# Kernel optimization log

Measured on AMD Instinct MI355X. Metric: run time of the kernel, lower is better.

## Reference

```python
import jax, jax.numpy as jnp
import numpy as np

D_MODEL, D_K, D_V, N_HEADS = 1024, 64, 64, 16
B, S = 8, 1024
NEG = -1e9
LN_EPS = 1e-5


def setup_inputs() -> dict:
    key = jax.random.key(0)
    ks = jax.random.split(key, 10)
    scale = 1.0 / np.sqrt(D_MODEL)
    return {
        "Q_in": jax.random.normal(ks[0], (B, S, D_MODEL), jnp.float32),
        "K_in": jax.random.normal(ks[1], (B, S, D_MODEL), jnp.float32),
        "V_in": jax.random.normal(ks[2], (B, S, D_MODEL), jnp.float32),
        "mask": jax.random.randint(ks[3], (B, S, S), 0, 2).astype(bool),
        "W_Q": jax.random.normal(ks[4], (D_MODEL, N_HEADS * D_K), jnp.float32) * scale,
        "W_K": jax.random.normal(ks[5], (D_MODEL, N_HEADS * D_K), jnp.float32) * scale,
        "W_V": jax.random.normal(ks[6], (D_MODEL, N_HEADS * D_V), jnp.float32) * scale,
        "W_fc": jax.random.normal(ks[7], (N_HEADS * D_V, D_MODEL), jnp.float32) * scale,
        "ln_gamma": jnp.ones((D_MODEL,), jnp.float32),
        "ln_beta": jnp.zeros((D_MODEL,), jnp.float32),
    }


def reference(Q_in, K_in, V_in, mask, W_Q, W_K, W_V, W_fc, ln_gamma, ln_beta):
    b = Q_in.shape[0]
    # projections -> (B, H, S, d)
    Q = (Q_in @ W_Q).reshape(b, -1, N_HEADS, D_K).transpose(0, 2, 1, 3)
    K = (K_in @ W_K).reshape(b, -1, N_HEADS, D_K).transpose(0, 2, 1, 3)
    V = (V_in @ W_V).reshape(b, -1, N_HEADS, D_V).transpose(0, 2, 1, 3)
    # scores (B, H, Sq, Sk)
    scores = jnp.einsum("bhqd,bhkd->bhqk", Q, K) / np.sqrt(D_K)
    scores = jnp.where(mask[:, None, :, :], NEG, scores)
    attn = jax.nn.softmax(scores, axis=-1)
    context = jnp.einsum("bhqk,bhkd->bhqd", attn, V)
    context = context.transpose(0, 2, 1, 3).reshape(b, -1, N_HEADS * D_V)
    out = context @ W_fc + Q_in  # residual
    mu = jnp.mean(out, axis=-1, keepdims=True)
    var = jnp.var(out, axis=-1, keepdims=True)
    out = (out - mu) * jax.lax.rsqrt(var + LN_EPS) * ln_gamma + ln_beta
    return out, attn
```

## Files before the change

### kernel.cpp

```cpp
#include <hip/hip_runtime.h>
#include <stdint.h>

typedef unsigned short u16;
typedef float f32x4 __attribute__((ext_vector_type(4)));
typedef short s16x8 __attribute__((ext_vector_type(8)));

constexpr int B  = 8;
constexpr int S  = 1024;
constexpr int DM = 1024;
constexpr int H  = 16;
constexpr int M  = B * S;
constexpr float NEGINF = -1e9f;

__device__ __forceinline__ u16 f2bf(float f) {
    union { float f; uint32_t u; } v; v.f = f;
    uint32_t u = v.u;
    uint32_t r = 0x7FFFu + ((u >> 16) & 1u);
    return (u16)((u + r) >> 16);
}

__device__ __forceinline__ void gload16(const u16* g, u16* l) {
    __builtin_amdgcn_global_load_lds(
        (const __attribute__((address_space(1))) unsigned int*)g,
        (__attribute__((address_space(3))) unsigned int*)l, 16, 0, 0);
}

__global__ void cvt_all(const float* __restrict__ q, const float* __restrict__ k,
                        const float* __restrict__ v,
                        u16* __restrict__ xq, u16* __restrict__ xk, u16* __restrict__ xv) {
    const float* in; u16* out;
    if (blockIdx.y == 0)      { in = q; out = xq; }
    else if (blockIdx.y == 1) { in = k; out = xk; }
    else                      { in = v; out = xv; }
    int i = (blockIdx.x * 256 + threadIdx.x) * 4;
    float4 val = *(const float4*)(in + i);
    ushort4 o;
    o.x = f2bf(val.x); o.y = f2bf(val.y); o.z = f2bf(val.z); o.w = f2bf(val.w);
    *(ushort4*)(out + i) = o;
}

__global__ void transpose_all(const float* __restrict__ w0, const float* __restrict__ w1,
                              const float* __restrict__ w2, const float* __restrict__ w3,
                              u16* __restrict__ o0, u16* __restrict__ o1,
                              u16* __restrict__ o2, u16* __restrict__ o3) {
    const float* W; u16* Wt;
    switch (blockIdx.z) {
        case 0:  W = w0; Wt = o0; break;
        case 1:  W = w1; Wt = o1; break;
        case 2:  W = w2; Wt = o2; break;
        default: W = w3; Wt = o3; break;
    }
    __shared__ float tile[32][33];
    int n0 = blockIdx.x * 32, k0 = blockIdx.y * 32;
    int tx = threadIdx.x & 31, ty = threadIdx.x >> 5;
#pragma unroll
    for (int r = 0; r < 4; ++r)
        tile[ty + r*8][tx] = W[(size_t)(k0 + ty + r*8) * DM + n0 + tx];
    __syncthreads();
#pragma unroll
    for (int r = 0; r < 4; ++r)
        Wt[(size_t)(n0 + ty + r*8) * DM + k0 + tx] = f2bf(tile[tx][ty + r*8]);
}

template<int EPI>
__global__ __launch_bounds__(256, 2)
void gemm_bt(const u16* __restrict__ A, const u16* __restrict__ Bt,
             void* __restrict__ Cv, const float* __restrict__ resid)
{
    __shared__ u16 As[128 * 32];
    __shared__ u16 Bs[128 * 32];
    const int m0 = blockIdx.y * 128;
    const int n0 = blockIdx.x * 128;
    const int t = threadIdx.x;
    const int lane = t & 63;
    const int wid = t >> 6;
    const int wm = (wid >> 1) * 64;
    const int wn = (wid & 1) * 64;
    const int lr = lane & 15;
    const int lg = lane >> 4;

    const u16* Ag = A  + (size_t)(m0 + (t >> 2)) * 1024 + (t & 3) * 8;
    const u16* Bg = Bt + (size_t)(n0 + (t >> 2)) * 1024 + (t & 3) * 8;
    u16* Al = As + t * 8;
    u16* Bl = Bs + t * 8;

    f32x4 acc[4][4] = {};

    for (int kt = 0; kt < 32; ++kt) {
        const int ko = kt * 32;
        __syncthreads();
        gload16(Ag + ko,            Al);
        gload16(Ag + 64*1024 + ko,  Al + 64*32);
        gload16(Bg + ko,            Bl);
        gload16(Bg + 64*1024 + ko,  Bl + 64*32);
        __syncthreads();
        s16x8 af[4], bfr[4];
#pragma unroll
        for (int m = 0; m < 4; ++m)
            af[m] = *(const s16x8*)(As + (wm + m*16 + lr) * 32 + lg * 8);
#pragma unroll
        for (int n = 0; n < 4; ++n)
            bfr[n] = *(const s16x8*)(Bs + (wn + n*16 + lr) * 32 + lg * 8);
#pragma unroll
        for (int m = 0; m < 4; ++m)
#pragma unroll
            for (int n = 0; n < 4; ++n)
                acc[m][n] = __builtin_amdgcn_mfma_f32_16x16x32_bf16(af[m], bfr[n], acc[m][n], 0, 0, 0);
    }

#pragma unroll
    for (int m = 0; m < 4; ++m) {
#pragma unroll
        for (int n = 0; n < 4; ++n) {
            const int rg0 = m0 + wm + m*16 + lg*4;
            const int cg  = n0 + wn + n*16 + lr;
            if constexpr (EPI == 0) {
                u16* C = (u16*)Cv;
#pragma unroll
                for (int r = 0; r < 4; ++r)
                    C[(size_t)(rg0 + r) * 1024 + cg] = f2bf(acc[m][n][r]);
            } else if constexpr (EPI == 1) {
                u16* C = (u16*)Cv;
                const int bb = rg0 >> 10;
                const int s0 = rg0 & 1023;
                const int hh = cg >> 6;
                const int dd = cg & 63;
                ushort4 pk;
                pk.x = f2bf(acc[m][n][0]); pk.y = f2bf(acc[m][n][1]);
                pk.z = f2bf(acc[m][n][2]); pk.w = f2bf(acc[m][n][3]);
                *(ushort4*)(C + (size_t)((bb*16 + hh)*64 + dd) * 1024 + s0) = pk;
            } else {
                float* C = (float*)Cv;
#pragma unroll
                for (int r = 0; r < 4; ++r) {
                    size_t idx = (size_t)(rg0 + r) * 1024 + cg;
                    C[idx] = acc[m][n][r] + resid[idx];
                }
            }
        }
    }
}

__global__ __launch_bounds__(256, 2)
void attn_fused(const u16* __restrict__ Qp, const u16* __restrict__ Kp,
                const void* __restrict__ maskp, const u16* __restrict__ Vt,
                float* __restrict__ attn, u16* __restrict__ ctx)
{
    const int h  = blockIdx.x;
    const int q0 = blockIdx.y * 32;
    const int b  = blockIdx.z;
    const int t = threadIdx.x;
    const int lane = t & 63;
    const int w = t >> 6;
    const int lr = lane & 15;
    const int lg = lane >> 4;

    constexpr int PLD = 1032;
    __shared__ u16 Plds[32 * PLD];
    __shared__ float redA[4][32];
    __shared__ float redB[4][32];

    uint32_t orv = 0;
    const uint32_t* mw = (const uint32_t*)maskp;
#pragma unroll
    for (int i = 0; i < 64; ++i) orv |= mw[i];
    const bool mask_bytes = (orv > 1u);

    s16x8 qf[2][2];
#pragma unroll
    for (int mq = 0; mq < 2; ++mq)
#pragma unroll
        for (int ks = 0; ks < 2; ++ks)
            qf[mq][ks] = *(const s16x8*)(Qp + (size_t)(b*S + q0 + mq*16 + lr) * DM + h*64 + ks*32 + lg*8);

    f32x4 acc[2][16];
#pragma unroll
    for (int nk = 0; nk < 16; ++nk) {
        const int sk = w*256 + nk*16 + lr;
        const u16* kb = Kp + (size_t)(b*S + sk) * DM + h*64 + lg*8;
        s16x8 kf0 = *(const s16x8*)(kb);
        s16x8 kf1 = *(const s16x8*)(kb + 32);
        f32x4 c0 = {};
        c0 = __builtin_amdgcn_mfma_f32_16x16x32_bf16(qf[0][0], kf0, c0, 0, 0, 0);
        c0 = __builtin_amdgcn_mfma_f32_16x16x32_bf16(qf[0][1], kf1, c0, 0, 0, 0);
        acc[0][nk] = c0;
        f32x4 c1 = {};
        c1 = __builtin_amdgcn_mfma_f32_16x16x32_bf16(qf[1][0], kf0, c1, 0, 0, 0);
        c1 = __builtin_amdgcn_mfma_f32_16x16x32_bf16(qf[1][1], kf1, c1, 0, 0, 0);
        acc[1][nk] = c1;
    }

    const size_t mbase = (size_t)b * S * S;
#pragma unroll
    for (int mq = 0; mq < 2; ++mq) {
#pragma unroll
        for (int r = 0; r < 4; ++r) {
            const int q = q0 + mq*16 + lg*4 + r;
            const size_t roff = mbase + (size_t)q * S + w*256 + lr;
#pragma unroll
            for (int nk = 0; nk < 16; ++nk) {
                int mv;
                if (mask_bytes) mv = ((const uint8_t*)maskp)[roff + nk*16];
                else            mv = ((const int*)maskp)[roff + nk*16];
                float s = acc[mq][nk][r] * 0.125f;
                acc[mq][nk][r] = mv ? NEGINF : s;
            }
        }
    }

    float rmax[2][4];
#pragma unroll
    for (int mq = 0; mq < 2; ++mq)
#pragma unroll
        for (int r = 0; r < 4; ++r) {
            float m = acc[mq][0][r];
#pragma unroll
            for (int nk = 1; nk < 16; ++nk) m = fmaxf(m, acc[mq][nk][r]);
#pragma unroll
            for (int d = 1; d < 16; d <<= 1) m = fmaxf(m, __shfl_xor(m, d, 64));
            rmax[mq][r] = m;
        }
    if (lr == 0) {
#pragma unroll
        for (int mq = 0; mq < 2; ++mq)
#pragma unroll
            for (int r = 0; r < 4; ++r)
                redA[w][mq*16 + lg*4 + r] = rmax[mq][r];
    }
    __syncthreads();
#pragma unroll
    for (int mq = 0; mq < 2; ++mq)
#pragma unroll
        for (int r = 0; r < 4; ++r) {
            const int row = mq*16 + lg*4 + r;
            rmax[mq][r] = fmaxf(fmaxf(redA[0][row], redA[1][row]),
                                fmaxf(redA[2][row], redA[3][row]));
        }

#pragma unroll
    for (int mq = 0; mq < 2; ++mq)
#pragma unroll
        for (int r = 0; r < 4; ++r) {
            float sme = 0.f;
#pragma unroll
            for (int nk = 0; nk < 16; ++nk) {
                float p = __expf(acc[mq][nk][r] - rmax[mq][r]);
                acc[mq][nk][r] = p;
                sme += p;
            }
#pragma unroll
            for (int d = 1; d < 16; d <<= 1) sme += __shfl_xor(sme, d, 64);
            if (lr == 0) redB[w][mq*16 + lg*4 + r] = sme;
        }
    __syncthreads();

#pragma unroll
    for (int mq = 0; mq < 2; ++mq)
#pragma unroll
        for (int r = 0; r < 4; ++r) {
            const int row = mq*16 + lg*4 + r;
            const float inv = 1.0f / (redB[0][row] + redB[1][row] + redB[2][row] + redB[3][row]);
#pragma unroll
            for (int nk = 0; nk < 16; ++nk) {
                float p = acc[mq][nk][r] * inv;
                acc[mq][nk][r] = p;
                Plds[row * PLD + w*256 + nk*16 + lr] = f2bf(p);
            }
        }
    __syncthreads();

    float* ab = attn + (size_t)(b*H + h) * S * S;
#pragma unroll
    for (int mq = 0; mq < 2; ++mq)
#pragma unroll
        for (int r = 0; r < 4; ++r) {
            float* arow = ab + (size_t)(q0 + mq*16 + lg*4 + r) * S + w*256 + lr;
#pragma unroll
            for (int nk = 0; nk < 16; ++nk)
                arow[nk*16] = acc[mq][nk][r];
        }

    const u16* vb = Vt + (size_t)(b*H + h) * 64 * S + (size_t)(w*16 + lr) * S;
    f32x4 pacc[2] = {};
    for (int kt = 0; kt < 32; ++kt) {
        const int k0 = kt*32 + lg*8;
        s16x8 vf = *(const s16x8*)(vb + k0);
#pragma unroll
        for (int mq = 0; mq < 2; ++mq) {
            s16x8 af = *(const s16x8*)(Plds + (mq*16 + lr) * PLD + k0);
            pacc[mq] = __builtin_amdgcn_mfma_f32_16x16x32_bf16(af, vf, pacc[mq], 0, 0, 0);
        }
    }
#pragma unroll
    for (int mq = 0; mq < 2; ++mq)
#pragma unroll
        for (int r = 0; r < 4; ++r)
            ctx[(size_t)(b*S + q0 + mq*16 + lg*4 + r) * DM + h*64 + w*16 + lr] = f2bf(pacc[mq][r]);
}

__global__ __launch_bounds__(256)
void layernorm(const float* __restrict__ x, const float* __restrict__ gamma,
               const float* __restrict__ beta, float* __restrict__ out)
{
    const int row = blockIdx.x;
    const int t = threadIdx.x;
    const float* xr = x + (size_t)row * DM;
    float4 v = *(const float4*)(xr + t*4);
    float s  = v.x + v.y + v.z + v.w;
    float s2 = v.x*v.x + v.y*v.y + v.z*v.z + v.w*v.w;
#pragma unroll
    for (int d = 1; d < 64; d <<= 1) {
        s  += __shfl_xor(s,  d, 64);
        s2 += __shfl_xor(s2, d, 64);
    }
    __shared__ float ls[4], ls2[4];
    if ((t & 63) == 0) { ls[t >> 6] = s; ls2[t >> 6] = s2; }
    __syncthreads();
    s  = ls[0] + ls[1] + ls[2] + ls[3];
    s2 = ls2[0] + ls2[1] + ls2[2] + ls2[3];
    const float mu  = s * (1.0f / DM);
    const float var = s2 * (1.0f / DM) - mu * mu;
    const float rs  = rsqrtf(var + 1e-5f);
    float4 g  = *(const float4*)(gamma + t*4);
    float4 bb = *(const float4*)(beta  + t*4);
    float4 o;
    o.x = (v.x - mu) * rs * g.x + bb.x;
    o.y = (v.y - mu) * rs * g.y + bb.y;
    o.z = (v.z - mu) * rs * g.z + bb.z;
    o.w = (v.w - mu) * rs * g.w + bb.w;
    *(float4*)(out + (size_t)row * DM + t*4) = o;
}

extern "C" void kernel_launch(void* const* d_in, const int* in_sizes, int n_in,
                              void* d_out, int out_size, void* d_ws, size_t ws_size,
                              hipStream_t stream) {
    const float* Qin  = (const float*)d_in[0];
    const float* Kin  = (const float*)d_in[1];
    const float* Vin  = (const float*)d_in[2];
    const void*  mask = d_in[3];
    const float* Wq   = (const float*)d_in[4];
    const float* Wk   = (const float*)d_in[5];
    const float* Wv   = (const float*)d_in[6];
    const float* Wfc  = (const float*)d_in[7];
    const float* gam  = (const float*)d_in[8];
    const float* bet  = (const float*)d_in[9];

    float* out  = (float*)d_out;
    float* attn = (float*)d_out + (size_t)M * DM;

    char* ws = (char*)d_ws;
    constexpr size_t SZ_X = (size_t)M * DM * 2;
    constexpr size_t SZ_W = (size_t)DM * DM * 2;
    u16* Xq  = (u16*)(ws);
    u16* Xk  = (u16*)(ws + SZ_X);
    u16* Xv  = (u16*)(ws + 2*SZ_X);
    u16* WqT = (u16*)(ws + 3*SZ_X);
    u16* WkT = (u16*)(ws + 3*SZ_X + SZ_W);
    u16* WvT = (u16*)(ws + 3*SZ_X + 2*SZ_W);
    u16* WfT = (u16*)(ws + 3*SZ_X + 3*SZ_W);
    u16* Qp  = (u16*)(ws + 3*SZ_X + 4*SZ_W);
    u16* Kp  = (u16*)(ws + 4*SZ_X + 4*SZ_W);
    u16* Vt  = (u16*)(ws + 5*SZ_X + 4*SZ_W);
    float* preLN = (float*)(ws);
    u16*   Ctx   = (u16*)(ws + 2*SZ_X);

    dim3 blk(256);
    cvt_all<<<dim3(M * DM / 1024, 3), blk, 0, stream>>>(Qin, Kin, Vin, Xq, Xk, Xv);
    transpose_all<<<dim3(32, 32, 4), blk, 0, stream>>>(Wq, Wk, Wv, Wfc, WqT, WkT, WvT, WfT);

    gemm_bt<0><<<dim3(8, 64), blk, 0, stream>>>(Xq, WqT, Qp, nullptr);
    gemm_bt<0><<<dim3(8, 64), blk, 0, stream>>>(Xk, WkT, Kp, nullptr);
    gemm_bt<1><<<dim3(8, 64), blk, 0, stream>>>(Xv, WvT, Vt, nullptr);

    attn_fused<<<dim3(H, S / 32, B), blk, 0, stream>>>(Qp, Kp, mask, Vt, attn, Ctx);

    gemm_bt<2><<<dim3(8, 64), blk, 0, stream>>>(Ctx, WfT, preLN, Qin);
    layernorm<<<dim3(M), blk, 0, stream>>>(preLN, gam, bet, out);
}
```

Baseline: 568.3 us.

## Restructure attention block to 16 queries with transposed scores and vectorized stores

Each attention block now handles 16 query rows instead of 32. The score MFMA swaps its operands so each lane holds 4 consecutive key columns, which lets mask reads become uchar4/int4 loads and attn writes become float4 stores instead of scalar strided accesses. P·V is split along the key dimension across the 4 waves, with partial context sums reduced through LDS. LDS use per block drops and the launch bound targets 3 blocks per CU. The cost is that K is re-read twice as often and there is an extra cross-wave reduction step.

Result: faster. 547.0 us (-3.7%).

```diff
diff --git a/kernel.cpp b/kernel.cpp
--- a/kernel.cpp
+++ b/kernel.cpp
@@ -141,13 +141,13 @@
     }
 }
 
-__global__ __launch_bounds__(256, 2)
+__global__ __launch_bounds__(256, 3)
 void attn_fused(const u16* __restrict__ Qp, const u16* __restrict__ Kp,
                 const void* __restrict__ maskp, const u16* __restrict__ Vt,
                 float* __restrict__ attn, u16* __restrict__ ctx)
 {
     const int h  = blockIdx.x;
-    const int q0 = blockIdx.y * 32;
+    const int q0 = blockIdx.y * 16;
     const int b  = blockIdx.z;
     const int t = threadIdx.x;
     const int lane = t & 63;
@@ -155,10 +155,10 @@
     const int lr = lane & 15;
     const int lg = lane >> 4;
 
-    constexpr int PLD = 1032;
-    __shared__ u16 Plds[32 * PLD];
-    __shared__ float redA[4][32];
-    __shared__ float redB[4][32];
+    __shared__ u16  Pl[4][16][264];
+    __shared__ float ctxp[4][16][64];
+    __shared__ float redA[4][16];
+    __shared__ float redB[4][16];
 
     uint32_t orv = 0;
     const uint32_t* mw = (const uint32_t*)maskp;
@@ -166,136 +166,116 @@
     for (int i = 0; i < 64; ++i) orv |= mw[i];
     const bool mask_bytes = (orv > 1u);
 
-    s16x8 qf[2][2];
-#pragma unroll
-    for (int mq = 0; mq < 2; ++mq)
-#pragma unroll
-        for (int ks = 0; ks < 2; ++ks)
-            qf[mq][ks] = *(const s16x8*)(Qp + (size_t)(b*S + q0 + mq*16 + lr) * DM + h*64 + ks*32 + lg*8);
-
-    f32x4 acc[2][16];
+    const u16* qb = Qp + (size_t)(b*S + q0 + lr) * DM + h*64 + lg*8;
+    s16x8 qf0 = *(const s16x8*)(qb);
+    s16x8 qf1 = *(const s16x8*)(qb + 32);
+
+    f32x4 p[16];
 #pragma unroll
     for (int nk = 0; nk < 16; ++nk) {
-        const int sk = w*256 + nk*16 + lr;
-        const u16* kb = Kp + (size_t)(b*S + sk) * DM + h*64 + lg*8;
+        const u16* kb = Kp + (size_t)(b*S + w*256 + nk*16 + lr) * DM + h*64 + lg*8;
         s16x8 kf0 = *(const s16x8*)(kb);
         s16x8 kf1 = *(const s16x8*)(kb + 32);
-        f32x4 c0 = {};
-        c0 = __builtin_amdgcn_mfma_f32_16x16x32_bf16(qf[0][0], kf0, c0, 0, 0, 0);
-        c0 = __builtin_amdgcn_mfma_f32_16x16x32_bf16(qf[0][1], kf1, c0, 0, 0, 0);
-        acc[0][nk] = c0;
-        f32x4 c1 = {};
-        c1 = __builtin_amdgcn_mfma_f32_16x16x32_bf16(qf[1][0], kf0, c1, 0, 0, 0);
-        c1 = __builtin_amdgcn_mfma_f32_16x16x32_bf16(qf[1][1], kf1, c1, 0, 0, 0);
-        acc[1][nk] = c1;
-    }
-
-    const size_t mbase = (size_t)b * S * S;
-#pragma unroll
-    for (int mq = 0; mq < 2; ++mq) {
-#pragma unroll
-        for (int r = 0; r < 4; ++r) {
-            const int q = q0 + mq*16 + lg*4 + r;
-            const size_t roff = mbase + (size_t)q * S + w*256 + lr;
-#pragma unroll
-            for (int nk = 0; nk < 16; ++nk) {
-                int mv;
-                if (mask_bytes) mv = ((const uint8_t*)maskp)[roff + nk*16];
-                else            mv = ((const int*)maskp)[roff + nk*16];
-                float s = acc[mq][nk][r] * 0.125f;
-                acc[mq][nk][r] = mv ? NEGINF : s;
-            }
+        f32x4 c = {};
+        c = __builtin_amdgcn_mfma_f32_16x16x32_bf16(kf0, qf0, c, 0, 0, 0);
+        c = __builtin_amdgcn_mfma_f32_16x16x32_bf16(kf1, qf1, c, 0, 0, 0);
+        p[nk] = c;
+    }
+
+    const size_t mrow = (size_t)b * S * S + (size_t)(q0 + lr) * S;
+#pragma unroll
+    for (int nk = 0; nk < 16; ++nk) {
+        const size_t off = mrow + w*256 + nk*16 + lg*4;
+        int m0, m1, m2, m3;
+        if (mask_bytes) {
+            uchar4 mb = *(const uchar4*)((const uint8_t*)maskp + off);
+            m0 = mb.x; m1 = mb.y; m2 = mb.z; m3 = mb.w;
+        } else {
+            int4 mi = *(const int4*)((const int*)maskp + off);
+            m0 = mi.x; m1 = mi.y; m2 = mi.z; m3 = mi.w;
         }
-    }
-
-    float rmax[2][4];
-#pragma unroll
-    for (int mq = 0; mq < 2; ++mq)
-#pragma unroll
-        for (int r = 0; r < 4; ++r) {
-            float m = acc[mq][0][r];
-#pragma unroll
-            for (int nk = 1; nk < 16; ++nk) m = fmaxf(m, acc[mq][nk][r]);
-#pragma unroll
-            for (int d = 1; d < 16; d <<= 1) m = fmaxf(m, __shfl_xor(m, d, 64));
-            rmax[mq][r] = m;
+        p[nk][0] = m0 ? NEGINF : p[nk][0] * 0.125f;
+        p[nk][1] = m1 ? NEGINF : p[nk][1] * 0.125f;
+        p[nk][2] = m2 ? NEGINF : p[nk][2] * 0.125f;
+        p[nk][3] = m3 ? NEGINF : p[nk][3] * 0.125f;
+    }
+
+    f32x4 vm = p[0];
+#pragma unroll
+    for (int nk = 1; nk < 16; ++nk) {
+        vm[0] = fmaxf(vm[0], p[nk][0]); vm[1] = fmaxf(vm[1], p[nk][1]);
+        vm[2] = fmaxf(vm[2], p[nk][2]); vm[3] = fmaxf(vm[3], p[nk][3]);
+    }
+    float hm = fmaxf(fmaxf(vm[0], vm[1]), fmaxf(vm[2], vm[3]));
+    hm = fmaxf(hm, __shfl_xor(hm, 16, 64));
+    hm = fmaxf(hm, __shfl_xor(hm, 32, 64));
+    if (lane < 16) redA[w][lr] = hm;
+    __syncthreads();
+    const float fm = fmaxf(fmaxf(redA[0][lr], redA[1][lr]),
+                           fmaxf(redA[2][lr], redA[3][lr]));
+
+    float hs = 0.f;
+#pragma unroll
+    for (int nk = 0; nk < 16; ++nk) {
+        p[nk][0] = __expf(p[nk][0] - fm);
+        p[nk][1] = __expf(p[nk][1] - fm);
+        p[nk][2] = __expf(p[nk][2] - fm);
+        p[nk][3] = __expf(p[nk][3] - fm);
+        hs += p[nk][0] + p[nk][1] + p[nk][2] + p[nk][3];
+    }
+    hs += __shfl_xor(hs, 16, 64);
+    hs += __shfl_xor(hs, 32, 64);
+    if (lane < 16) redB[w][lr] = hs;
+    __syncthreads();
+    const float inv = 1.0f / (redB[0][lr] + redB[1][lr] + redB[2][lr] + redB[3][lr]);
+
+    float* arow = attn + (size_t)(b*H + h) * S * S + (size_t)(q0 + lr) * S + w*256 + lg*4;
+#pragma unroll
+    for (int nk = 0; nk < 16; ++nk) {
+        p[nk][0] *= inv; p[nk][1] *= inv; p[nk][2] *= inv; p[nk][3] *= inv;
+        float4 st; st.x = p[nk][0]; st.y = p[nk][1]; st.z = p[nk][2]; st.w = p[nk][3];
+        *(float4*)(arow + nk*16) = st;
+        uint2 pk;
+        pk.x = (uint32_t)f2bf(p[nk][0]) | ((uint32_t)f2bf(p[nk][1]) << 16);
+        pk.y = (uint32_t)f2bf(p[nk][2]) | ((uint32_t)f2bf(p[nk][3]) << 16);
+        *(uint2*)&Pl[w][lr][nk*16 + lg*4] = pk;
+    }
+    __syncthreads();
+
+    const u16* vb = Vt + (size_t)(b*H + h) * 64 * S + w*256 + lg*8;
+    f32x4 pacc[4] = {};
+#pragma unroll
+    for (int kt = 0; kt < 8; ++kt) {
+        s16x8 af = *(const s16x8*)&Pl[w][lr][kt*32 + lg*8];
+#pragma unroll
+        for (int d0 = 0; d0 < 4; ++d0) {
+            s16x8 vf = *(const s16x8*)(vb + (size_t)(d0*16 + lr) * S + kt*32);
+            pacc[d0] = __builtin_amdgcn_mfma_f32_16x16x32_bf16(af, vf, pacc[d0], 0, 0, 0);
         }
-    if (lr == 0) {
-#pragma unroll
-        for (int mq = 0; mq < 2; ++mq)
-#pragma unroll
-            for (int r = 0; r < 4; ++r)
-                redA[w][mq*16 + lg*4 + r] = rmax[mq][r];
-    }
-    __syncthreads();
-#pragma unroll
-    for (int mq = 0; mq < 2; ++mq)
-#pragma unroll
-        for (int r = 0; r < 4; ++r) {
-            const int row = mq*16 + lg*4 + r;
-            rmax[mq][r] = fmaxf(fmaxf(redA[0][row], redA[1][row]),
-                                fmaxf(redA[2][row], redA[3][row]));
-        }
-
-#pragma unroll
-    for (int mq = 0; mq < 2; ++mq)
-#pragma unroll
-        for (int r = 0; r < 4; ++r) {
-            float sme = 0.f;
-#pragma unroll
-            for (int nk = 0; nk < 16; ++nk) {
-                float p = __expf(acc[mq][nk][r] - rmax[mq][r]);
-                acc[mq][nk][r] = p;
-                sme += p;
-            }
-#pragma unroll
-            for (int d = 1; d < 16; d <<= 1) sme += __shfl_xor(sme, d, 64);
-            if (lr == 0) redB[w][mq*16 + lg*4 + r] = sme;
-        }
-    __syncthreads();
-
-#pragma unroll
-    for (int mq = 0; mq < 2; ++mq)
-#pragma unroll
-        for (int r = 0; r < 4; ++r) {
-            const int row = mq*16 + lg*4 + r;
-            const float inv = 1.0f / (redB[0][row] + redB[1][row] + redB[2][row] + redB[3][row]);
-#pragma unroll
-            for (int nk = 0; nk < 16; ++nk) {
-                float p = acc[mq][nk][r] * inv;
-                acc[mq][nk][r] = p;
-                Plds[row * PLD + w*256 + nk*16 + lr] = f2bf(p);
-            }
-        }
-    __syncthreads();
-
-    float* ab = attn + (size_t)(b*H + h) * S * S;
-#pragma unroll
-    for (int mq = 0; mq < 2; ++mq)
-#pragma unroll
-        for (int r = 0; r < 4; ++r) {
-            float* arow = ab + (size_t)(q0 + mq*16 + lg*4 + r) * S + w*256 + lr;
-#pragma unroll
-            for (int nk = 0; nk < 16; ++nk)
-                arow[nk*16] = acc[mq][nk][r];
-        }
-
-    const u16* vb = Vt + (size_t)(b*H + h) * 64 * S + (size_t)(w*16 + lr) * S;
-    f32x4 pacc[2] = {};
-    for (int kt = 0; kt < 32; ++kt) {
-        const int k0 = kt*32 + lg*8;
-        s16x8 vf = *(const s16x8*)(vb + k0);
-#pragma unroll
-        for (int mq = 0; mq < 2; ++mq) {
-            s16x8 af = *(const s16x8*)(Plds + (mq*16 + lr) * PLD + k0);
-            pacc[mq] = __builtin_amdgcn_mfma_f32_16x16x32_bf16(af, vf, pacc[mq], 0, 0, 0);
-        }
-    }
-#pragma unroll
-    for (int mq = 0; mq < 2; ++mq)
+    }
+#pragma unroll
+    for (int d0 = 0; d0 < 4; ++d0)
 #pragma unroll
         for (int r = 0; r < 4; ++r)
-            ctx[(size_t)(b*S + q0 + mq*16 + lg*4 + r) * DM + h*64 + w*16 + lr] = f2bf(pacc[mq][r]);
+            ctxp[w][lg*4 + r][d0*16 + lr] = pacc[d0][r];
+    __syncthreads();
+
+    {
+        const int q  = t >> 4;
+        const int d4 = (t & 15) * 4;
+        float4 s0 = *(const float4*)&ctxp[0][q][d4];
+        float4 s1 = *(const float4*)&ctxp[1][q][d4];
+        float4 s2 = *(const float4*)&ctxp[2][q][d4];
+        float4 s3 = *(const float4*)&ctxp[3][q][d4];
+        float4 sm;
+        sm.x = s0.x + s1.x + s2.x + s3.x;
+        sm.y = s0.y + s1.y + s2.y + s3.y;
+        sm.z = s0.z + s1.z + s2.z + s3.z;
+        sm.w = s0.w + s1.w + s2.w + s3.w;
+        ushort4 o;
+        o.x = f2bf(sm.x); o.y = f2bf(sm.y); o.z = f2bf(sm.z); o.w = f2bf(sm.w);
+        *(ushort4*)(ctx + (size_t)(b*S + q0 + q) * DM + h*64 + d4) = o;
+    }
 }
 
 __global__ __launch_bounds__(256)
@@ -372,7 +352,7 @@
     gemm_bt<0><<<dim3(8, 64), blk, 0, stream>>>(Xk, WkT, Kp, nullptr);
     gemm_bt<1><<<dim3(8, 64), blk, 0, stream>>>(Xv, WvT, Vt, nullptr);
 
-    attn_fused<<<dim3(H, S / 32, B), blk, 0, stream>>>(Qp, Kp, mask, Vt, attn, Ctx);
+    attn_fused<<<dim3(H, S / 16, B), blk, 0, stream>>>(Qp, Kp, mask, Vt, attn, Ctx);
 
     gemm_bt<2><<<dim3(8, 64), blk, 0, stream>>>(Ctx, WfT, preLN, Qin);
     layernorm<<<dim3(M), blk, 0, stream>>>(preLN, gam, bet, out);
```
